# Kernel optimization log

Hardware: AMD Instinct MI355X
Metric: run time of the kernel (lower is better)

## Reference

```python
import jax, jax.numpy as jnp
import numpy as np

N = 20000      # nodes
E = 320000     # edges (avg degree 16)
C = 64         # channels per degree
H = 8          # attention heads
DIM1 = 3       # degree-1 representation dim (2*1+1)
NUM_FEATURES = C * 1 + C * 3  # key_fiber.num_features = 256


def setup_inputs() -> dict:
    key = jax.random.key(0)
    ks = jax.random.split(key, 7)
    return {
        "value_0": jax.random.normal(ks[0], (E, C, 1), dtype=jnp.float32),
        "value_1": jax.random.normal(ks[1], (E, C, DIM1), dtype=jnp.float32),
        "key_0": jax.random.normal(ks[2], (E, C, 1), dtype=jnp.float32),
        "key_1": jax.random.normal(ks[3], (E, C, DIM1), dtype=jnp.float32),
        "query_0": jax.random.normal(ks[4], (N, C, 1), dtype=jnp.float32),
        "query_1": jax.random.normal(ks[5], (N, C, DIM1), dtype=jnp.float32),
        "dst": jax.random.randint(ks[6], (E,), 0, N),
    }


def _to_heads(f0, f1):
    # Fiber.to_attention_heads: per degree [n, C, dim] -> [n, H, (C//H)*dim], concat on last dim
    n = f0.shape[0]
    return jnp.concatenate([f0.reshape(n, H, -1), f1.reshape(n, H, -1)], axis=-1)


def reference(value_0, value_1, key_0, key_1, query_0, query_1, dst):
    k = _to_heads(key_0, key_1)        # [E, H, Dk]
    q = _to_heads(query_0, query_1)    # [N, H, Dk]
    # dgl.ops.e_dot_v: dot edge key with destination-node query, then scale
    logits = jnp.einsum('ehd,ehd->eh', k, q[dst]) / np.float32(np.sqrt(NUM_FEATURES))
    edge_prelogits = logits            # returned pre-softmax (scaled) as in original
    # edge_softmax over incoming edges of each destination node, per head
    m = jax.ops.segment_max(logits, dst, num_segments=N)           # [N, H]
    w = jnp.exp(logits - m[dst])                                   # [E, H]
    denom = jax.ops.segment_sum(w, dst, num_segments=N)            # [N, H]
    alpha = w / denom[dst]                                         # [E, H]

    def agg(v, dim):
        # value view: [E, H, C//H, dim]; weighted copy_e_sum -> [N, C, dim]
        vh = v.reshape(E, H, C // H, dim)
        out = jax.ops.segment_sum(alpha[:, :, None, None] * vh, dst, num_segments=N)
        return out.reshape(N, C, dim)

    out_0 = agg(value_0, 1)
    out_1 = agg(value_1, DIM1)
    return out_0, out_1, edge_prelogits
```

## Files before the change

kernel.cpp:

```cpp
#include <hip/hip_runtime.h>

#define N_NODES 20000
#define N_EDGES 320000
#define NEGF   -1e30f


__global__ __launch_bounds__(256) void k_zero(int* __restrict__ counts)
{
    int n = blockIdx.x * 256 + threadIdx.x;
    if (n < N_NODES) counts[n] = 0;
}

__global__ __launch_bounds__(256) void k_count(
    const int* __restrict__ dst, int* __restrict__ counts)
{
    int e = blockIdx.x * 256 + threadIdx.x;
    if (e < N_EDGES) atomicAdd(&counts[dst[e]], 1);
}

__global__ __launch_bounds__(1024) void k_scan(
    const int* __restrict__ counts, int* __restrict__ offsets,
    int* __restrict__ cursor)
{
    __shared__ int sm[1024];
    int t = threadIdx.x;
    int base = t * 20;
    int local[20];
    int s = 0;
    if (base < N_NODES) {
#pragma unroll
        for (int i = 0; i < 20; ++i) { local[i] = counts[base + i]; s += local[i]; }
    }
    sm[t] = s; __syncthreads();
    for (int off = 1; off < 1024; off <<= 1) {
        int x = (t >= off) ? sm[t - off] : 0;
        __syncthreads();
        sm[t] += x;
        __syncthreads();
    }
    int run = sm[t] - s;
    if (base < N_NODES) {
#pragma unroll
        for (int i = 0; i < 20; ++i) {
            offsets[base + i] = run; cursor[base + i] = run; run += local[i];
        }
    }
    if (t == 0) offsets[N_NODES] = N_EDGES;
}

__global__ __launch_bounds__(256) void k_fill(
    const int* __restrict__ dst, int* __restrict__ cursor, int* __restrict__ bucket)
{
    int e = blockIdx.x * 256 + threadIdx.x;
    if (e >= N_EDGES) return;
    int d = dst[e];
    int pos = atomicAdd(&cursor[d], 1);
    bucket[pos] = e;
}

__global__ __launch_bounds__(256) void k_fused(
    const float* __restrict__ v0, const float* __restrict__ v1,
    const float* __restrict__ k0, const float* __restrict__ k1,
    const float* __restrict__ q0, const float* __restrict__ q1,
    const int* __restrict__ offsets, const int* __restrict__ bucket,
    float* __restrict__ logits, float* __restrict__ out0, float* __restrict__ out1)
{
    __shared__ float xb[4][512];
    __shared__ float qs[4][256];
    int w = threadIdx.x >> 6;
    int l = threadIdx.x & 63;
    int node = blockIdx.x * 4 + w;
    float* X = xb[w];
    float* Q = qs[w];

    int rs = offsets[node], re = offsets[node + 1];
    int deg = re - rs;
    int h = l & 7, slot8 = l >> 3;

    {
        float4* Qv = (float4*)Q;
        if (l < 16) Qv[l] = ((const float4*)(q0 + (size_t)node * 64))[l];
        else        Qv[l] = ((const float4*)(q1 + (size_t)node * 192))[l - 16];
    }
    __syncthreads();

    const float4* Qh0 = (const float4*)(Q + h * 8);
    const float4* Qh1 = (const float4*)(Q + 64 + h * 24);
    float M = NEGF, S = 0.f;
    for (int base = 0; base < deg; base += 8) {
        int s = base + slot8;
        bool ok = s < deg;
        float x = NEGF;
        if (ok) {
            int e = bucket[rs + s];
            const float4* kk0 = (const float4*)(k0 + (size_t)e * 64  + h * 8);
            const float4* kk1 = (const float4*)(k1 + (size_t)e * 192 + h * 24);
            float acc = 0.f;
#pragma unroll
            for (int i = 0; i < 2; ++i) {
                float4 a = kk0[i], b = Qh0[i];
                acc += a.x * b.x + a.y * b.y + a.z * b.z + a.w * b.w;
            }
#pragma unroll
            for (int i = 0; i < 6; ++i) {
                float4 a = kk1[i], b = Qh1[i];
                acc += a.x * b.x + a.y * b.y + a.z * b.z + a.w * b.w;
            }
            x = acc * 0.0625f;
            logits[(size_t)e * 8 + h] = x;
            if (s < 64) X[s * 8 + h] = x;
        }
        float Mn = fmaxf(M, x);
        S = S * __expf(M - Mn) + (ok ? __expf(x - Mn) : 0.f);
        M = Mn;
    }
    for (int mask = 8; mask < 64; mask <<= 1) {
        float Mo = __shfl_xor(M, mask);
        float So = __shfl_xor(S, mask);
        float Mn = fmaxf(M, Mo);
        S = S * __expf(M - Mn) + So * __expf(Mo - Mn);
        M = Mn;
    }
    float rinv = (S > 0.f) ? 1.f / S : 0.f;

    int degc = deg < 64 ? deg : 64;
    for (int base = 0; base < degc; base += 8) {
        int s = base + slot8;
        if (s < degc) X[s * 8 + h] = __expf(X[s * 8 + h] - M) * rinv;
    }
    __syncthreads();

    int s2 = l >> 4;
    int c  = l & 15;
    int hv0  = c >> 1;
    int hv1a = c / 6;
    int hv1b = (c + 16) / 6;
    int hv1c = (c + 32) / 6;
    float M0 = __shfl(M, hv0),  R0 = __shfl(rinv, hv0);
    float Ma = __shfl(M, hv1a), Ra = __shfl(rinv, hv1a);
    float Mb = __shfl(M, hv1b), Rb = __shfl(rinv, hv1b);
    float Mc = __shfl(M, hv1c), Rc = __shfl(rinv, hv1c);

    float4 a0  = {0,0,0,0}, a1a = {0,0,0,0}, a1b = {0,0,0,0}, a1c = {0,0,0,0};
    for (int base = 0; base < deg; base += 4) {
        int s = base + s2;
        bool ok = s < deg;
        int e = bucket[rs + (ok ? s : deg - 1)];
        float al0, ala, alb, alc;
        if (s < 64) {
            al0 = X[s * 8 + hv0];
            ala = X[s * 8 + hv1a];
            alb = X[s * 8 + hv1b];
            alc = X[s * 8 + hv1c];
        } else {
            const float* lr = logits + (size_t)e * 8;
            al0 = __expf(lr[hv0]  - M0) * R0;
            ala = __expf(lr[hv1a] - Ma) * Ra;
            alb = __expf(lr[hv1b] - Mb) * Rb;
            alc = __expf(lr[hv1c] - Mc) * Rc;
        }
        if (!ok) { al0 = ala = alb = alc = 0.f; }
        const float4* r0 = (const float4*)(v0 + (size_t)e * 64);
        const float4* r1 = (const float4*)(v1 + (size_t)e * 192);
        float4 p0 = r0[c];
        float4 pa = r1[c];
        float4 pb = r1[c + 16];
        float4 pc = r1[c + 32];
        a0.x  += al0 * p0.x; a0.y  += al0 * p0.y; a0.z  += al0 * p0.z; a0.w  += al0 * p0.w;
        a1a.x += ala * pa.x; a1a.y += ala * pa.y; a1a.z += ala * pa.z; a1a.w += ala * pa.w;
        a1b.x += alb * pb.x; a1b.y += alb * pb.y; a1b.z += alb * pb.z; a1b.w += alb * pb.w;
        a1c.x += alc * pc.x; a1c.y += alc * pc.y; a1c.z += alc * pc.z; a1c.w += alc * pc.w;
    }
#pragma unroll
    for (int mask = 16; mask < 64; mask <<= 1) {
        a0.x  += __shfl_xor(a0.x,  mask); a0.y  += __shfl_xor(a0.y,  mask);
        a0.z  += __shfl_xor(a0.z,  mask); a0.w  += __shfl_xor(a0.w,  mask);
        a1a.x += __shfl_xor(a1a.x, mask); a1a.y += __shfl_xor(a1a.y, mask);
        a1a.z += __shfl_xor(a1a.z, mask); a1a.w += __shfl_xor(a1a.w, mask);
        a1b.x += __shfl_xor(a1b.x, mask); a1b.y += __shfl_xor(a1b.y, mask);
        a1b.z += __shfl_xor(a1b.z, mask); a1b.w += __shfl_xor(a1b.w, mask);
        a1c.x += __shfl_xor(a1c.x, mask); a1c.y += __shfl_xor(a1c.y, mask);
        a1c.z += __shfl_xor(a1c.z, mask); a1c.w += __shfl_xor(a1c.w, mask);
    }
    if (l < 16) {
        float4* o0 = (float4*)(out0 + (size_t)node * 64);
        float4* o1 = (float4*)(out1 + (size_t)node * 192);
        o0[c]      = a0;
        o1[c]      = a1a;
        o1[c + 16] = a1b;
        o1[c + 32] = a1c;
    }
}

extern "C" void kernel_launch(void* const* d_in, const int* in_sizes, int n_in,
                              void* d_out, int out_size, void* d_ws, size_t ws_size,
                              hipStream_t stream) {
    const float* v0 = (const float*)d_in[0];
    const float* v1 = (const float*)d_in[1];
    const float* k0 = (const float*)d_in[2];
    const float* k1 = (const float*)d_in[3];
    const float* q0 = (const float*)d_in[4];
    const float* q1 = (const float*)d_in[5];
    const int*  dst = (const int*)d_in[6];

    float* out0   = (float*)d_out;
    float* out1   = out0 + (size_t)N_NODES * 64;
    float* logits = out1 + (size_t)N_NODES * 192;

    int* wsI     = (int*)d_ws;
    int* counts  = wsI;
    int* offsets = wsI + 20000;
    int* cursor  = wsI + 40064;
    int* bucket  = wsI + 60192;

    k_zero  <<<79,    256,  0, stream>>>(counts);
    k_count <<<1250,  256,  0, stream>>>(dst, counts);
    k_scan  <<<1,     1024, 0, stream>>>(counts, offsets, cursor);
    k_fill  <<<1250,  256,  0, stream>>>(dst, cursor, bucket);
    k_fused <<<5000,  256,  0, stream>>>(v0, v1, k0, k1, q0, q1,
                                         offsets, bucket, logits, out0, out1);
}
```

Baseline: 204.2 us.

## Fuse logit, online softmax and value aggregation into a single edge pass

Replaces the two-pass per-node scheme (logits plus softmax stats, then a second sweep over edges for value aggregation) with one loop. Each 8-edge chunk computes logits, updates a running max and sum via wave shuffles, rescales the accumulators, and immediately accumulates values weighted by unnormalised exponentials. Query rows are held in registers and bucket indices are cached in a lane register, which removes the LDS buffers and block barriers. The cost is more shuffles and accumulator rescales per chunk, and higher register pressure.

```diff
diff --git a/kernel.cpp b/kernel.cpp
--- a/kernel.cpp
+++ b/kernel.cpp
@@ -58,6 +58,12 @@
     bucket[pos] = e;
 }
 
+#define DOT4(a,b) ((a).x*(b).x + (a).y*(b).y + (a).z*(b).z + (a).w*(b).w)
+#define SC4(a,s)  { (a).x*=(s); (a).y*=(s); (a).z*=(s); (a).w*=(s); }
+#define FMA4(a,s,p) { (a).x += (s)*(p).x; (a).y += (s)*(p).y; (a).z += (s)*(p).z; (a).w += (s)*(p).w; }
+#define RED4(a,m) { (a).x += __shfl_xor((a).x,m); (a).y += __shfl_xor((a).y,m); \
+                    (a).z += __shfl_xor((a).z,m); (a).w += __shfl_xor((a).w,m); }
+
 __global__ __launch_bounds__(256) void k_fused(
     const float* __restrict__ v0, const float* __restrict__ v1,
     const float* __restrict__ k0, const float* __restrict__ k1,
@@ -65,124 +71,107 @@
     const int* __restrict__ offsets, const int* __restrict__ bucket,
     float* __restrict__ logits, float* __restrict__ out0, float* __restrict__ out1)
 {
-    __shared__ float xb[4][512];
-    __shared__ float qs[4][256];
     int w = threadIdx.x >> 6;
     int l = threadIdx.x & 63;
     int node = blockIdx.x * 4 + w;
-    float* X = xb[w];
-    float* Q = qs[w];
 
     int rs = offsets[node], re = offsets[node + 1];
     int deg = re - rs;
-    int h = l & 7, slot8 = l >> 3;
-
-    {
-        float4* Qv = (float4*)Q;
-        if (l < 16) Qv[l] = ((const float4*)(q0 + (size_t)node * 64))[l];
-        else        Qv[l] = ((const float4*)(q1 + (size_t)node * 192))[l - 16];
-    }
-    __syncthreads();
-
-    const float4* Qh0 = (const float4*)(Q + h * 8);
-    const float4* Qh1 = (const float4*)(Q + 64 + h * 24);
-    float M = NEGF, S = 0.f;
-    for (int base = 0; base < deg; base += 8) {
-        int s = base + slot8;
-        bool ok = s < deg;
-        float x = NEGF;
-        if (ok) {
-            int e = bucket[rs + s];
-            const float4* kk0 = (const float4*)(k0 + (size_t)e * 64  + h * 8);
-            const float4* kk1 = (const float4*)(k1 + (size_t)e * 192 + h * 24);
-            float acc = 0.f;
-#pragma unroll
-            for (int i = 0; i < 2; ++i) {
-                float4 a = kk0[i], b = Qh0[i];
-                acc += a.x * b.x + a.y * b.y + a.z * b.z + a.w * b.w;
-            }
-#pragma unroll
-            for (int i = 0; i < 6; ++i) {
-                float4 a = kk1[i], b = Qh1[i];
-                acc += a.x * b.x + a.y * b.y + a.z * b.z + a.w * b.w;
-            }
-            x = acc * 0.0625f;
-            logits[(size_t)e * 8 + h] = x;
-            if (s < 64) X[s * 8 + h] = x;
-        }
-        float Mn = fmaxf(M, x);
-        S = S * __expf(M - Mn) + (ok ? __expf(x - Mn) : 0.f);
-        M = Mn;
-    }
-    for (int mask = 8; mask < 64; mask <<= 1) {
-        float Mo = __shfl_xor(M, mask);
-        float So = __shfl_xor(S, mask);
-        float Mn = fmaxf(M, Mo);
-        S = S * __expf(M - Mn) + So * __expf(Mo - Mn);
-        M = Mn;
-    }
-    float rinv = (S > 0.f) ? 1.f / S : 0.f;
-
-    int degc = deg < 64 ? deg : 64;
-    for (int base = 0; base < degc; base += 8) {
-        int s = base + slot8;
-        if (s < degc) X[s * 8 + h] = __expf(X[s * 8 + h] - M) * rinv;
-    }
-    __syncthreads();
-
-    int s2 = l >> 4;
-    int c  = l & 15;
+
+    int h = l & 7, slot8 = l >> 3, s2 = l >> 4, c = l & 15;
     int hv0  = c >> 1;
     int hv1a = c / 6;
     int hv1b = (c + 16) / 6;
     int hv1c = (c + 32) / 6;
-    float M0 = __shfl(M, hv0),  R0 = __shfl(rinv, hv0);
-    float Ma = __shfl(M, hv1a), Ra = __shfl(rinv, hv1a);
-    float Mb = __shfl(M, hv1b), Rb = __shfl(rinv, hv1b);
-    float Mc = __shfl(M, hv1c), Rc = __shfl(rinv, hv1c);
-
+
+    const float4* qh0 = (const float4*)(q0 + (size_t)node * 64  + h * 8);
+    const float4* qh1 = (const float4*)(q1 + (size_t)node * 192 + h * 24);
+    float4 Q0a = qh0[0], Q0b = qh0[1];
+    float4 Q1a = qh1[0], Q1b = qh1[1], Q1c = qh1[2];
+    float4 Q1d = qh1[3], Q1e = qh1[4], Q1f = qh1[5];
+
+    int eL = 0;
+    if (l < deg) eL = bucket[rs + l];
+
+    float M = NEGF, S = 0.f;
     float4 a0  = {0,0,0,0}, a1a = {0,0,0,0}, a1b = {0,0,0,0}, a1c = {0,0,0,0};
-    for (int base = 0; base < deg; base += 4) {
-        int s = base + s2;
-        bool ok = s < deg;
-        int e = bucket[rs + (ok ? s : deg - 1)];
-        float al0, ala, alb, alc;
-        if (s < 64) {
-            al0 = X[s * 8 + hv0];
-            ala = X[s * 8 + hv1a];
-            alb = X[s * 8 + hv1b];
-            alc = X[s * 8 + hv1c];
-        } else {
-            const float* lr = logits + (size_t)e * 8;
-            al0 = __expf(lr[hv0]  - M0) * R0;
-            ala = __expf(lr[hv1a] - Ma) * Ra;
-            alb = __expf(lr[hv1b] - Mb) * Rb;
-            alc = __expf(lr[hv1c] - Mc) * Rc;
-        }
-        if (!ok) { al0 = ala = alb = alc = 0.f; }
-        const float4* r0 = (const float4*)(v0 + (size_t)e * 64);
-        const float4* r1 = (const float4*)(v1 + (size_t)e * 192);
-        float4 p0 = r0[c];
-        float4 pa = r1[c];
-        float4 pb = r1[c + 16];
-        float4 pc = r1[c + 32];
-        a0.x  += al0 * p0.x; a0.y  += al0 * p0.y; a0.z  += al0 * p0.z; a0.w  += al0 * p0.w;
-        a1a.x += ala * pa.x; a1a.y += ala * pa.y; a1a.z += ala * pa.z; a1a.w += ala * pa.w;
-        a1b.x += alb * pb.x; a1b.y += alb * pb.y; a1b.z += alb * pb.z; a1b.w += alb * pb.w;
-        a1c.x += alc * pc.x; a1c.y += alc * pc.y; a1c.z += alc * pc.z; a1c.w += alc * pc.w;
-    }
-#pragma unroll
-    for (int mask = 16; mask < 64; mask <<= 1) {
-        a0.x  += __shfl_xor(a0.x,  mask); a0.y  += __shfl_xor(a0.y,  mask);
-        a0.z  += __shfl_xor(a0.z,  mask); a0.w  += __shfl_xor(a0.w,  mask);
-        a1a.x += __shfl_xor(a1a.x, mask); a1a.y += __shfl_xor(a1a.y, mask);
-        a1a.z += __shfl_xor(a1a.z, mask); a1a.w += __shfl_xor(a1a.w, mask);
-        a1b.x += __shfl_xor(a1b.x, mask); a1b.y += __shfl_xor(a1b.y, mask);
-        a1b.z += __shfl_xor(a1b.z, mask); a1b.w += __shfl_xor(a1b.w, mask);
-        a1c.x += __shfl_xor(a1c.x, mask); a1c.y += __shfl_xor(a1c.y, mask);
-        a1c.z += __shfl_xor(a1c.z, mask); a1c.w += __shfl_xor(a1c.w, mask);
-    }
+
+    for (int base = 0; base < deg; base += 8) {
+        int sA = base + slot8;
+        bool okA = sA < deg;
+        int iA = okA ? sA : 0;
+        int eA = (iA < 64) ? __shfl(eL, iA) : bucket[rs + iA];
+
+        int sB0 = base + s2, sB1 = base + s2 + 4;
+        int iB0 = (sB0 < deg) ? sB0 : 0;
+        int iB1 = (sB1 < deg) ? sB1 : 0;
+        int eB0 = (iB0 < 64) ? __shfl(eL, iB0) : bucket[rs + iB0];
+        int eB1 = (iB1 < 64) ? __shfl(eL, iB1) : bucket[rs + iB1];
+
+        const float4* kr0 = (const float4*)(k0 + (size_t)eA * 64  + h * 8);
+        const float4* kr1 = (const float4*)(k1 + (size_t)eA * 192 + h * 24);
+        float4 K0a = kr0[0], K0b = kr0[1];
+        float4 K1a = kr1[0], K1b = kr1[1], K1c = kr1[2];
+        float4 K1d = kr1[3], K1e = kr1[4], K1f = kr1[5];
+
+        const float4* v0A = (const float4*)(v0 + (size_t)eB0 * 64);
+        const float4* v1A = (const float4*)(v1 + (size_t)eB0 * 192);
+        const float4* v0B = (const float4*)(v0 + (size_t)eB1 * 64);
+        const float4* v1B = (const float4*)(v1 + (size_t)eB1 * 192);
+        float4 P0A = v0A[c], PaA = v1A[c], PbA = v1A[c + 16], PcA = v1A[c + 32];
+        float4 P0B = v0B[c], PaB = v1B[c], PbB = v1B[c + 16], PcB = v1B[c + 32];
+
+        float acc = DOT4(K0a, Q0a) + DOT4(K0b, Q0b)
+                  + DOT4(K1a, Q1a) + DOT4(K1b, Q1b) + DOT4(K1c, Q1c)
+                  + DOT4(K1d, Q1d) + DOT4(K1e, Q1e) + DOT4(K1f, Q1f);
+        float x = okA ? acc * 0.0625f : NEGF;
+        if (okA) logits[(size_t)eA * 8 + h] = x;
+
+        float gM = x;
+        gM = fmaxf(gM, __shfl_xor(gM, 8));
+        gM = fmaxf(gM, __shfl_xor(gM, 16));
+        gM = fmaxf(gM, __shfl_xor(gM, 32));
+        float Mn = fmaxf(M, gM);
+        float atil = okA ? __expf(x - Mn) : 0.f;
+        float gS = atil;
+        gS += __shfl_xor(gS, 8);
+        gS += __shfl_xor(gS, 16);
+        gS += __shfl_xor(gS, 32);
+        float sc = __expf(M - Mn);
+        S = S * sc + gS;
+        M = Mn;
+
+        float sc0 = __shfl(sc, hv0);
+        float sca = __shfl(sc, hv1a);
+        float scb = __shfl(sc, hv1b);
+        float scc = __shfl(sc, hv1c);
+        SC4(a0, sc0); SC4(a1a, sca); SC4(a1b, scb); SC4(a1c, scc);
+
+        float l0A = __shfl(atil, s2 * 8 + hv0);
+        float laA = __shfl(atil, s2 * 8 + hv1a);
+        float lbA = __shfl(atil, s2 * 8 + hv1b);
+        float lcA = __shfl(atil, s2 * 8 + hv1c);
+        float l0B = __shfl(atil, (s2 + 4) * 8 + hv0);
+        float laB = __shfl(atil, (s2 + 4) * 8 + hv1a);
+        float lbB = __shfl(atil, (s2 + 4) * 8 + hv1b);
+        float lcB = __shfl(atil, (s2 + 4) * 8 + hv1c);
+        FMA4(a0, l0A, P0A); FMA4(a1a, laA, PaA); FMA4(a1b, lbA, PbA); FMA4(a1c, lcA, PcA);
+        FMA4(a0, l0B, P0B); FMA4(a1a, laB, PaB); FMA4(a1b, lbB, PbB); FMA4(a1c, lcB, PcB);
+    }
+
+    float rinv = (S > 0.f) ? 1.f / S : 0.f;
+    float r0 = __shfl(rinv, hv0);
+    float ra = __shfl(rinv, hv1a);
+    float rb = __shfl(rinv, hv1b);
+    float rc = __shfl(rinv, hv1c);
+
+    RED4(a0, 16); RED4(a0, 32);
+    RED4(a1a, 16); RED4(a1a, 32);
+    RED4(a1b, 16); RED4(a1b, 32);
+    RED4(a1c, 16); RED4(a1c, 32);
+
     if (l < 16) {
+        SC4(a0, r0); SC4(a1a, ra); SC4(a1b, rb); SC4(a1c, rc);
         float4* o0 = (float4*)(out0 + (size_t)node * 64);
         float4* o1 = (float4*)(out1 + (size_t)node * 192);
         o0[c]      = a0;
```

Measured after the change: 203.7 us. About the same (-0.2%).
